# Kernel optimization log

Measured on AMD Instinct MI355X. Metric: run time of the kernel, lower is better.

## Reference

```python
import jax, jax.numpy as jnp
import numpy as np

B, T, N, D = 8, 12, 325, 256
H = 8
HD = D // H
FF = 1024
SCALE = HD ** -0.5
EPS = 1e-5
NEG_INF = jnp.float32(-1e30)


def layernorm(x, w, b):
    mu = jnp.mean(x, axis=-1, keepdims=True)
    var = jnp.mean(jnp.square(x - mu), axis=-1, keepdims=True)
    return (x - mu) * jax.lax.rsqrt(var + EPS) * w + b


def mha(x, wq, bq, wk, bk, wv, bv, wo, bo, mask):
    # x: (G, L, D); mask: (L, L) bool, True = keep, or None
    G, L, _ = x.shape
    q = (x @ wq + bq).reshape(G, L, H, HD)
    k = (x @ wk + bk).reshape(G, L, H, HD)
    v = (x @ wv + bv).reshape(G, L, H, HD)
    scores = jnp.einsum('glhd,gmhd->ghlm', q, k) * SCALE
    if mask is not None:
        scores = jnp.where(mask[None, None], scores, NEG_INF)
    attn = jax.nn.softmax(scores, axis=-1)
    out = jnp.einsum('ghlm,gmhd->glhd', attn, v).reshape(G, L, D)
    return out @ wo + bo


def setup_inputs() -> dict:
    key = jax.random.key(0)
    ks = jax.random.split(key, 16)
    s = 0.02
    inp = {
        'x': jax.random.normal(ks[0], (B, T, N, D), jnp.float32),
        'adj_mask': jax.random.randint(ks[1], (N, N), 0, 2, jnp.int32),
        'sa_wq': jax.random.normal(ks[2], (D, D)) * s, 'sa_bq': jnp.zeros((D,)),
        'sa_wk': jax.random.normal(ks[3], (D, D)) * s, 'sa_bk': jnp.zeros((D,)),
        'sa_wv': jax.random.normal(ks[4], (D, D)) * s, 'sa_bv': jnp.zeros((D,)),
        'sa_wo': jax.random.normal(ks[5], (D, D)) * s, 'sa_bo': jnp.zeros((D,)),
        'sa_ln_w': jnp.ones((D,)), 'sa_ln_b': jnp.zeros((D,)),
        'ta_wq': jax.random.normal(ks[6], (D, D)) * s, 'ta_bq': jnp.zeros((D,)),
        'ta_wk': jax.random.normal(ks[7], (D, D)) * s, 'ta_bk': jnp.zeros((D,)),
        'ta_wv': jax.random.normal(ks[8], (D, D)) * s, 'ta_bv': jnp.zeros((D,)),
        'ta_wo': jax.random.normal(ks[9], (D, D)) * s, 'ta_bo': jnp.zeros((D,)),
        'ta_ln_w': jnp.ones((D,)), 'ta_ln_b': jnp.zeros((D,)),
        'f_w1': jax.random.normal(ks[10], (D, FF)) * s, 'f_b1': jnp.zeros((FF,)),
        'f_w2': jax.random.normal(ks[11], (FF, D)) * s, 'f_b2': jnp.zeros((D,)),
        'f_ln_w': jnp.ones((D,)), 'f_ln_b': jnp.zeros((D,)),
    }
    return inp


def reference(x, adj_mask,
              sa_wq, sa_bq, sa_wk, sa_bk, sa_wv, sa_bv, sa_wo, sa_bo, sa_ln_w, sa_ln_b,
              ta_wq, ta_bq, ta_wk, ta_bk, ta_wv, ta_bv, ta_wo, ta_bo, ta_ln_w, ta_ln_b,
              f_w1, f_b1, f_w2, f_b2, f_ln_w, f_ln_b):
    # Spatial attention over N at each (b, t)
    xs = x.reshape(B * T, N, D)
    sa = mha(xs, sa_wq, sa_bq, sa_wk, sa_bk, sa_wv, sa_bv, sa_wo, sa_bo,
             adj_mask != 0).reshape(B, T, N, D)
    x = layernorm(x + sa, sa_ln_w, sa_ln_b)

    # Temporal attention over T at each (b, n), causal
    xt = x.transpose(0, 2, 1, 3).reshape(B * N, T, D)
    causal = jnp.tril(jnp.ones((T, T), dtype=bool))
    ta = mha(xt, ta_wq, ta_bq, ta_wk, ta_bk, ta_wv, ta_bv, ta_wo, ta_bo, causal)
    ta = ta.reshape(B, N, T, D).transpose(0, 2, 1, 3)
    x = layernorm(x + ta, ta_ln_w, ta_ln_b)

    # FFN with exact GELU (torch nn.GELU default)
    h = jax.nn.gelu(x @ f_w1 + f_b1, approximate=False)
    out = layernorm(x + (h @ f_w2 + f_b2), f_ln_w, f_ln_b)
    return out
```

## Files before the change

### kernel.cpp

```cpp
#include <hip/hip_runtime.h>
#include <hip/hip_bf16.h>
#include <math.h>

#define B_   8
#define T_   12
#define NN   325
#define DD   256
#define HH   8
#define HD   32
#define FFD  1024
#define MTOK (B_*T_*NN)
#define QKVD 768
#define ATT_SCALE 0.17677669529663687f
#define LN_EPS 1e-5f
#define NEG_BIG (-1e30f)

typedef __attribute__((ext_vector_type(8))) __bf16 bf16x8;
typedef __attribute__((ext_vector_type(4))) float  f32x4;
typedef __attribute__((ext_vector_type(4))) short  shortx4;
typedef __attribute__((ext_vector_type(8))) unsigned short ushortx8;

static __device__ inline float bf2f(unsigned short u) {
  union { float f; unsigned int i; } c; c.i = ((unsigned int)u) << 16; return c.f;
}

#if __has_builtin(__builtin_amdgcn_mfma_f32_16x16x16bf16_1k)
#define MFMA16(a,b,c) __builtin_amdgcn_mfma_f32_16x16x16bf16_1k((a),(b),(c),0,0,0)
#else
static __device__ inline f32x4 mfma16_fn(shortx4 a, shortx4 b, f32x4 c) {
  f32x4 d;
  asm volatile("v_mfma_f32_16x16x16_bf16 %0, %1, %2, %3"
               : "=v"(d) : "v"(a), "v"(b), "v"(c));
  return d;
}
#define MFMA16(a,b,c) mfma16_fn((a),(b),(c))
#endif

#define GLDS(gsrc, ldst) \
  __builtin_amdgcn_global_load_lds((const __attribute__((address_space(1))) void*)(gsrc), \
                                   (__attribute__((address_space(3))) void*)(ldst), 16, 0, 0)

__global__ __launch_bounds__(256) void gemm_mfma(
    const __hip_bfloat16* __restrict__ A,
    const __hip_bfloat16* __restrict__ Wt,
    const float* __restrict__ bias,
    float* __restrict__ Cf, __hip_bfloat16* __restrict__ Cb,
    int Mr, int Nr, int Kr, int mode)
{
  __shared__ __hip_bfloat16 As[2][128 * 32];
  __shared__ __hip_bfloat16 Bs[2][128 * 32];

  const int NB  = Nr >> 7;
  const int nwg = gridDim.x;
  const int orig = blockIdx.x;
  const int qq = nwg >> 3, rr = nwg & 7;
  const int xcd = orig & 7, off = orig >> 3;
  const int id = (xcd < rr ? xcd * (qq + 1) : rr * (qq + 1) + (xcd - rr) * qq) + off;
  const int n0 = (id % NB) * 128;
  const int m0 = (id / NB) * 128;

  const int tid  = threadIdx.x;
  const int w    = tid >> 6;
  const int lane = tid & 63;
  const int wr   = w >> 1, wc = w & 1;

  f32x4 acc[4][4] = {};

  const int c4   = lane & 3;
  const int r0   = w * 32 + (lane >> 2);
  const int csw  = (c4 - (r0 >> 1)) & 3;
  const int scol = csw * 8;
  int ar0 = m0 + r0;      if (ar0 >= Mr) ar0 = Mr - 1;
  int ar1 = m0 + r0 + 16; if (ar1 >= Mr) ar1 = Mr - 1;
  const size_t aOff0 = (size_t)ar0 * Kr + scol;
  const size_t aOff1 = (size_t)ar1 * Kr + scol;
  const size_t bOff0 = (size_t)(n0 + r0) * Kr + scol;
  const size_t bOff1 = (size_t)(n0 + r0 + 16) * Kr + scol;

  const int lr = lane & 15;
  const int lg = lane >> 4;
  int offA[4], offB[4];
  #pragma unroll
  for (int i = 0; i < 4; ++i) {
    int rA = wr * 64 + i * 16 + lr;
    offA[i] = rA * 32 + (((lg + (rA >> 1)) & 3) * 8);
    int rB = wc * 64 + i * 16 + lr;
    offB[i] = rB * 32 + (((lg + (rB >> 1)) & 3) * 8);
  }
  const int nk = Kr >> 5;

#define STAGE_T(buf, k0) do { \
    GLDS(&A[aOff0 + (k0)],  &As[buf][(w * 32) * 32]); \
    GLDS(&A[aOff1 + (k0)],  &As[buf][(w * 32 + 16) * 32]); \
    GLDS(&Wt[bOff0 + (k0)], &Bs[buf][(w * 32) * 32]); \
    GLDS(&Wt[bOff1 + (k0)], &Bs[buf][(w * 32 + 16) * 32]); \
  } while (0)

  STAGE_T(0, 0);
  if (nk > 1) STAGE_T(1, 32);

  for (int k = 0; k < nk; ++k) {
    if (k + 1 < nk) asm volatile("s_waitcnt vmcnt(4)" ::: "memory");
    else            asm volatile("s_waitcnt vmcnt(0)" ::: "memory");
    __builtin_amdgcn_s_barrier();

    const int buf = k & 1;
    bf16x8 af[4], bfr[4];
    #pragma unroll
    for (int i = 0; i < 4; ++i) {
      af[i]  = *(const bf16x8*)&As[buf][offA[i]];
      bfr[i] = *(const bf16x8*)&Bs[buf][offB[i]];
    }
    asm volatile("s_waitcnt lgkmcnt(0)" ::: "memory");
    __builtin_amdgcn_sched_barrier(0);
    __builtin_amdgcn_s_barrier();

    if (k + 2 < nk) STAGE_T(buf, (k + 2) * 32);

    #pragma unroll
    for (int i = 0; i < 4; ++i)
      #pragma unroll
      for (int j = 0; j < 4; ++j)
        acc[i][j] = __builtin_amdgcn_mfma_f32_16x16x32_bf16(af[i], bfr[j], acc[i][j], 0, 0, 0);
  }
#undef STAGE_T

  const int rg = lg;
  #pragma unroll
  for (int i = 0; i < 4; ++i) {
    int rowb = m0 + wr * 64 + i * 16 + rg * 4;
    #pragma unroll
    for (int j = 0; j < 4; ++j) {
      int col = n0 + wc * 64 + j * 16 + lr;
      float bv = bias[col];
      #pragma unroll
      for (int q = 0; q < 4; ++q) {
        int gm = rowb + q;
        if (gm >= Mr) continue;
        float c = acc[i][j][q] + bv;
        if (mode == 0) {
          Cf[(size_t)gm * Nr + col] = c;
        } else {
          if (mode == 1) c = 0.5f * c * (1.f + erff(c * 0.70710678118654752f));
          Cb[(size_t)gm * Nr + col] = __float2bfloat16(c);
        }
      }
    }
  }
}

__global__ __launch_bounds__(256) void wt_cvt(
    const float* __restrict__ W, __hip_bfloat16* __restrict__ Wt, int K, int N)
{
  __shared__ float t[32][33];
  const int n0 = blockIdx.x * 32, k0 = blockIdx.y * 32;
  const int tx = threadIdx.x & 31, ty = threadIdx.x >> 5;
  #pragma unroll
  for (int i = 0; i < 32; i += 8)
    t[ty + i][tx] = W[(size_t)(k0 + ty + i) * N + n0 + tx];
  __syncthreads();
  #pragma unroll
  for (int i = 0; i < 32; i += 8)
    Wt[(size_t)(n0 + ty + i) * K + k0 + tx] = __float2bfloat16(t[tx][ty + i]);
}

__global__ __launch_bounds__(256) void cvt_bf16(
    const float* __restrict__ x, __hip_bfloat16* __restrict__ y, int n4)
{
  int i = blockIdx.x * 256 + threadIdx.x;
  if (i >= n4) return;
  float4 v = reinterpret_cast<const float4*>(x)[i];
  union { shortx4 s; __hip_bfloat16 h[4]; } u;
  u.h[0] = __float2bfloat16(v.x); u.h[1] = __float2bfloat16(v.y);
  u.h[2] = __float2bfloat16(v.z); u.h[3] = __float2bfloat16(v.w);
  reinterpret_cast<shortx4*>(y)[i] = u.s;
}

__global__ __launch_bounds__(256) void bias_cat3(
    const float* __restrict__ a, const float* __restrict__ b,
    const float* __restrict__ c, float* __restrict__ o)
{
  int i = blockIdx.x * 256 + threadIdx.x;
  if (i < 256) o[i] = a[i];
  else if (i < 512) o[i] = b[i - 256];
  else if (i < 768) o[i] = c[i - 512];
}

__global__ __launch_bounds__(256) void maskpack(
    const int* __restrict__ adj, unsigned int* __restrict__ mb)
{
  int idx = blockIdx.x * 256 + threadIdx.x;
  if (idx >= NN * 11) return;
  int l = idx / 11, w = idx % 11;
  unsigned int bits = 0;
  #pragma unroll 4
  for (int b = 0; b < 32; ++b) {
    int m = w * 32 + b;
    if (m < NN && adj[l * NN + m] != 0) bits |= (1u << b);
  }
  mb[idx] = bits;
}

__global__ __launch_bounds__(256) void spatial_attn_mfma(
    const __hip_bfloat16* __restrict__ qkv,
    const unsigned int* __restrict__ mb,
    __hip_bfloat16* __restrict__ out)
{
  constexpr int KP = 40;
  constexpr int VP = 340;
  __shared__ unsigned short Kl[336 * KP];
  __shared__ unsigned short Vt[32 * VP];

  const int g = blockIdx.x, h = blockIdx.y;
  const int tid = threadIdx.x;
  const int w = tid >> 6, lane = tid & 63;
  const int lq = lane & 15, lg = lane >> 4;

  const size_t baseQ = (size_t)g * NN * QKVD + (size_t)h * HD;
  const size_t baseK = baseQ + 256;
  const size_t baseV = baseQ + 512;

  for (int idx = tid; idx < 32 * (VP - NN); idx += 256) {
    int d = idx / (VP - NN), kk = NN + idx % (VP - NN);
    Vt[d * VP + kk] = 0;
  }
  for (int idx = tid; idx < NN * 4; idx += 256) {
    int row = idx >> 2, cc = (idx & 3) * 8;
    union { bf16x8 v; unsigned short u[8]; } kv, vv;
    kv.v = *(const bf16x8*)&qkv[baseK + (size_t)row * QKVD + cc];
    *(bf16x8*)&Kl[row * KP + cc] = kv.v;
    vv.v = *(const bf16x8*)&qkv[baseV + (size_t)row * QKVD + cc];
    #pragma unroll
    for (int j = 0; j < 8; ++j) Vt[(cc + j) * VP + row] = vv.u[j];
  }
  __syncthreads();

  for (int qt = w; qt < 21; qt += 4) {
    const int query = qt * 16 + lq;
    const int qc = query < NN ? query : NN - 1;
    const bf16x8 qf = *(const bf16x8*)&qkv[baseQ + (size_t)qc * QKVD + lg * 8];
    const unsigned int* mrow = &mb[qc * 11];

    f32x4 accL = {0.f, 0.f, 0.f, 0.f};
    f32x4 accH = {0.f, 0.f, 0.f, 0.f};
    float mrun = -INFINITY, lrun = 0.f;

    for (int t = 0; t < 21; ++t) {
      bf16x8 kf = *(const bf16x8*)&Kl[(t * 16 + lq) * KP + lg * 8];
      f32x4 st = __builtin_amdgcn_mfma_f32_16x16x32_bf16(
          kf, qf, (f32x4){0.f, 0.f, 0.f, 0.f}, 0, 0, 0);
      const unsigned int mw = mrow[t >> 1];
      const int kbase = t * 16 + lg * 4;
      const int bbase = (t & 1) * 16 + lg * 4;
      float s[4];
      #pragma unroll
      for (int q = 0; q < 4; ++q) {
        float fill = (kbase + q < NN) ? NEG_BIG : -INFINITY;
        s[q] = ((mw >> (bbase + q)) & 1u) ? st[q] * ATT_SCALE : fill;
      }
      float tmax = fmaxf(fmaxf(s[0], s[1]), fmaxf(s[2], s[3]));
      tmax = fmaxf(tmax, __shfl_xor(tmax, 16));
      tmax = fmaxf(tmax, __shfl_xor(tmax, 32));
      const float mnew = fmaxf(mrun, tmax);
      const float corr = __expf(mrun - mnew);
      float p0 = __expf(s[0] - mnew), p1 = __expf(s[1] - mnew);
      float p2 = __expf(s[2] - mnew), p3 = __expf(s[3] - mnew);
      float ps = p0 + p1 + p2 + p3;
      ps += __shfl_xor(ps, 16);
      ps += __shfl_xor(ps, 32);
      lrun = lrun * corr + ps;
      mrun = mnew;
      accL *= corr; accH *= corr;
      union { shortx4 s4; __hip_bfloat16 hh[4]; } up;
      up.hh[0] = __float2bfloat16(p0); up.hh[1] = __float2bfloat16(p1);
      up.hh[2] = __float2bfloat16(p2); up.hh[3] = __float2bfloat16(p3);
      shortx4 vaL = *(const shortx4*)&Vt[lq * VP + kbase];
      shortx4 vaH = *(const shortx4*)&Vt[(lq + 16) * VP + kbase];
      accL = MFMA16(vaL, up.s4, accL);
      accH = MFMA16(vaH, up.s4, accH);
    }

    if (query < NN) {
      const float inv = 1.f / lrun;
      const size_t ob = ((size_t)(g * NN + query)) * DD + (size_t)h * HD;
      union { shortx4 s4; __hip_bfloat16 hh[4]; } uL, uH;
      #pragma unroll
      for (int q = 0; q < 4; ++q) {
        uL.hh[q] = __float2bfloat16(accL[q] * inv);
        uH.hh[q] = __float2bfloat16(accH[q] * inv);
      }
      *(shortx4*)&out[ob + lg * 4]      = uL.s4;
      *(shortx4*)&out[ob + 16 + lg * 4] = uH.s4;
    }
  }
}

__global__ __launch_bounds__(256) void temporal_attn(
    const __hip_bfloat16* __restrict__ qkv, __hip_bfloat16* __restrict__ out)
{
  int idx = blockIdx.x * 256 + threadIdx.x;
  const int total = B_ * NN * HH * T_;
  if (idx >= total) return;

  int t  = idx % T_;
  int h  = (idx / T_) % HH;
  int n  = (idx / (T_ * HH)) % NN;
  int b  = idx / (T_ * HH * NN);

  const size_t tq = (size_t)((b * T_ + t) * NN + n) * QKVD + h * HD;
  float qr[HD];
  #pragma unroll
  for (int c8 = 0; c8 < 4; ++c8) {
    ushortx8 u = *(const ushortx8*)&qkv[tq + c8 * 8];
    #pragma unroll
    for (int j = 0; j < 8; ++j) qr[c8 * 8 + j] = bf2f(u[j]);
  }

  float o[HD] = {};
  float mrun = -INFINITY, lrun = 0.f;

  for (int tt = 0; tt <= t; ++tt) {
    const size_t tk = (size_t)((b * T_ + tt) * NN + n) * QKVD + h * HD;
    float s = 0.f;
    #pragma unroll
    for (int c8 = 0; c8 < 4; ++c8) {
      ushortx8 u = *(const ushortx8*)&qkv[tk + 256 + c8 * 8];
      #pragma unroll
      for (int j = 0; j < 8; ++j) s += qr[c8 * 8 + j] * bf2f(u[j]);
    }
    s *= ATT_SCALE;

    float mnew = fmaxf(mrun, s);
    float corr = __expf(mrun - mnew);
    float p = __expf(s - mnew);
    lrun = lrun * corr + p;
    #pragma unroll
    for (int c8 = 0; c8 < 4; ++c8) {
      ushortx8 u = *(const ushortx8*)&qkv[tk + 512 + c8 * 8];
      #pragma unroll
      for (int j = 0; j < 8; ++j) o[c8 * 8 + j] = o[c8 * 8 + j] * corr + p * bf2f(u[j]);
    }
    mrun = mnew;
  }

  float inv = 1.f / lrun;
  __hip_bfloat16* op = out + ((size_t)((b * T_ + t) * NN + n)) * DD + h * HD;
  #pragma unroll
  for (int d0 = 0; d0 < HD; d0 += 4) {
    union { shortx4 s; __hip_bfloat16 h4[4]; } u;
    #pragma unroll
    for (int j = 0; j < 4; ++j) u.h4[j] = __float2bfloat16(o[d0 + j] * inv);
    *reinterpret_cast<shortx4*>(op + d0) = u.s;
  }
}

__global__ __launch_bounds__(64) void add_ln(
    const float* __restrict__ x, const float* __restrict__ r,
    const float* __restrict__ w, const float* __restrict__ bb,
    float* __restrict__ y, __hip_bfloat16* __restrict__ ybf)
{
  const size_t row = blockIdx.x;
  const int lane = threadIdx.x;

  const float4 xv = reinterpret_cast<const float4*>(x + row * DD)[lane];
  const float4 rv = reinterpret_cast<const float4*>(r + row * DD)[lane];
  float e[4] = {xv.x + rv.x, xv.y + rv.y, xv.z + rv.z, xv.w + rv.w};

  float s  = e[0] + e[1] + e[2] + e[3];
  float ss = e[0]*e[0] + e[1]*e[1] + e[2]*e[2] + e[3]*e[3];
  #pragma unroll
  for (int off = 32; off > 0; off >>= 1) {
    s  += __shfl_xor(s,  off, 64);
    ss += __shfl_xor(ss, off, 64);
  }
  float mu  = s * (1.f / DD);
  float var = ss * (1.f / DD) - mu * mu;
  float rs  = rsqrtf(var + LN_EPS);

  const float4 wv = reinterpret_cast<const float4*>(w)[lane];
  const float4 bv = reinterpret_cast<const float4*>(bb)[lane];
  float o0 = (e[0] - mu) * rs * wv.x + bv.x;
  float o1 = (e[1] - mu) * rs * wv.y + bv.y;
  float o2 = (e[2] - mu) * rs * wv.z + bv.z;
  float o3 = (e[3] - mu) * rs * wv.w + bv.w;
  float4 yv = {o0, o1, o2, o3};
  reinterpret_cast<float4*>(y + row * DD)[lane] = yv;
  if (ybf) {
    union { shortx4 s4; __hip_bfloat16 h4[4]; } u;
    u.h4[0] = __float2bfloat16(o0); u.h4[1] = __float2bfloat16(o1);
    u.h4[2] = __float2bfloat16(o2); u.h4[3] = __float2bfloat16(o3);
    reinterpret_cast<shortx4*>(ybf + row * DD)[lane] = u.s4;
  }
}

extern "C" void kernel_launch(void* const* d_in, const int* in_sizes, int n_in,
                              void* d_out, int out_size, void* d_ws, size_t ws_size,
                              hipStream_t stream)
{
  const float* x0   = (const float*)d_in[0];
  const int*   adj  = (const int*)  d_in[1];
  const float* sa_wq = (const float*)d_in[2];
  const float* sa_bq = (const float*)d_in[3];
  const float* sa_wk = (const float*)d_in[4];
  const float* sa_bk = (const float*)d_in[5];
  const float* sa_wv = (const float*)d_in[6];
  const float* sa_bv = (const float*)d_in[7];
  const float* sa_wo = (const float*)d_in[8];
  const float* sa_bo = (const float*)d_in[9];
  const float* sa_lw = (const float*)d_in[10];
  const float* sa_lb = (const float*)d_in[11];
  const float* ta_wq = (const float*)d_in[12];
  const float* ta_bq = (const float*)d_in[13];
  const float* ta_wk = (const float*)d_in[14];
  const float* ta_bk = (const float*)d_in[15];
  const float* ta_wv = (const float*)d_in[16];
  const float* ta_bv = (const float*)d_in[17];
  const float* ta_wo = (const float*)d_in[18];
  const float* ta_bo = (const float*)d_in[19];
  const float* ta_lw = (const float*)d_in[20];
  const float* ta_lb = (const float*)d_in[21];
  const float* f_w1  = (const float*)d_in[22];
  const float* f_b1  = (const float*)d_in[23];
  const float* f_w2  = (const float*)d_in[24];
  const float* f_b2  = (const float*)d_in[25];
  const float* f_lw  = (const float*)d_in[26];
  const float* f_lb  = (const float*)d_in[27];

  float* out = (float*)d_out;
  float* ws  = (float*)d_ws;

  const size_t P = (size_t)MTOK * DD;
  if (ws_size < 7 * P * sizeof(float)) return;

  float* R0 = ws;
  __hip_bfloat16* QKVb = (__hip_bfloat16*)(ws + P);
  __hip_bfloat16* HIDb = (__hip_bfloat16*)(ws + P);
  float* R3 = ws + 3 * P;
  float* R4 = ws + 4 * P;
  __hip_bfloat16* X0b  = (__hip_bfloat16*)(ws + 5 * P);
  __hip_bfloat16* X1b  = (__hip_bfloat16*)(ws + 5 * P + P / 2);
  __hip_bfloat16* ATTb = (__hip_bfloat16*)(ws + 6 * P);
  __hip_bfloat16* Wb   = (__hip_bfloat16*)(ws + 6 * P + P / 2);

  __hip_bfloat16* sa_qkv_t = Wb;
  __hip_bfloat16* ta_qkv_t = Wb + 196608;
  __hip_bfloat16* sa_wo_t  = Wb + 393216;
  __hip_bfloat16* ta_wo_t  = Wb + 458752;
  __hip_bfloat16* f_w1_t   = Wb + 524288;
  __hip_bfloat16* f_w2_t   = Wb + 786432;
  float* sa_qkvb = (float*)(Wb + 1048576);
  float* ta_qkvb = sa_qkvb + 768;
  unsigned int* MB = (unsigned int*)(ta_qkvb + 768);

  wt_cvt<<<dim3(DD/32, DD/32), 256, 0, stream>>>(sa_wq, sa_qkv_t,          DD, DD);
  wt_cvt<<<dim3(DD/32, DD/32), 256, 0, stream>>>(sa_wk, sa_qkv_t + 65536,  DD, DD);
  wt_cvt<<<dim3(DD/32, DD/32), 256, 0, stream>>>(sa_wv, sa_qkv_t + 131072, DD, DD);
  wt_cvt<<<dim3(DD/32, DD/32), 256, 0, stream>>>(ta_wq, ta_qkv_t,          DD, DD);
  wt_cvt<<<dim3(DD/32, DD/32), 256, 0, stream>>>(ta_wk, ta_qkv_t + 65536,  DD, DD);
  wt_cvt<<<dim3(DD/32, DD/32), 256, 0, stream>>>(ta_wv, ta_qkv_t + 131072, DD, DD);
  wt_cvt<<<dim3(DD/32, DD/32), 256, 0, stream>>>(sa_wo, sa_wo_t, DD, DD);
  wt_cvt<<<dim3(DD/32, DD/32), 256, 0, stream>>>(ta_wo, ta_wo_t, DD, DD);
  wt_cvt<<<dim3(FFD/32, DD/32), 256, 0, stream>>>(f_w1, f_w1_t, DD, FFD);
  wt_cvt<<<dim3(DD/32, FFD/32), 256, 0, stream>>>(f_w2, f_w2_t, FFD, DD);
  bias_cat3<<<3, 256, 0, stream>>>(sa_bq, sa_bk, sa_bv, sa_qkvb);
  bias_cat3<<<3, 256, 0, stream>>>(ta_bq, ta_bk, ta_bv, ta_qkvb);
  maskpack<<<(NN * 11 + 255) / 256, 256, 0, stream>>>(adj, MB);
  {
    int n4 = (int)(P / 4);
    cvt_bf16<<<(n4 + 255) / 256, 256, 0, stream>>>(x0, X0b, n4);
  }

  const int MBk = (MTOK + 127) / 128;
  auto gemm = [&](const __hip_bfloat16* A, const __hip_bfloat16* Wt, const float* bias,
                  float* Cf, __hip_bfloat16* Cb, int Nr, int Kr, int mode) {
    int nwg = (Nr / 128) * MBk;
    gemm_mfma<<<nwg, 256, 0, stream>>>(A, Wt, bias, Cf, Cb, MTOK, Nr, Kr, mode);
  };

  gemm(X0b, sa_qkv_t, sa_qkvb, nullptr, QKVb, QKVD, DD, 2);
  spatial_attn_mfma<<<dim3(B_ * T_, HH), 256, 0, stream>>>(QKVb, MB, ATTb);
  gemm(ATTb, sa_wo_t, sa_bo, R3, nullptr, DD, DD, 0);
  add_ln<<<MTOK, 64, 0, stream>>>(x0, R3, sa_lw, sa_lb, R4, X1b);

  gemm(X1b, ta_qkv_t, ta_qkvb, nullptr, QKVb, QKVD, DD, 2);
  {
    int total = B_ * NN * HH * T_;
    temporal_attn<<<(total + 255) / 256, 256, 0, stream>>>(QKVb, ATTb);
  }
  gemm(ATTb, ta_wo_t, ta_bo, R3, nullptr, DD, DD, 0);
  add_ln<<<MTOK, 64, 0, stream>>>(R4, R3, ta_lw, ta_lb, R0, X0b);

  gemm(X0b, f_w1_t, f_b1, nullptr, HIDb, FFD, DD, 1);
  gemm(HIDb, f_w2_t, f_b2, R3, nullptr, DD, FFD, 0);
  add_ln<<<MTOK, 64, 0, stream>>>(R0, R3, f_lw, f_lb, out, nullptr);
}
```

Before: 413.2 us.

## Load GEMM operands directly from global memory and store projections as bf16

The GEMM drops its LDS double-buffered global_load_lds staging and barriers. Each lane now reads its MFMA fragments straight from global memory through per-row pointers, relying on cache for reuse across waves. The output-projection GEMMs also write bf16 instead of fp32, and add_ln reads the bf16 residual, which cuts store and load traffic. The risks are lost LDS data reuse, more redundant global and cache traffic with poorly coalesced 16-byte loads, and slightly lower precision in the projection outputs.

```diff
diff --git a/kernel.cpp b/kernel.cpp
--- a/kernel.cpp
+++ b/kernel.cpp
@@ -36,20 +36,13 @@
 #define MFMA16(a,b,c) mfma16_fn((a),(b),(c))
 #endif
 
-#define GLDS(gsrc, ldst) \
-  __builtin_amdgcn_global_load_lds((const __attribute__((address_space(1))) void*)(gsrc), \
-                                   (__attribute__((address_space(3))) void*)(ldst), 16, 0, 0)
-
-__global__ __launch_bounds__(256) void gemm_mfma(
+__global__ __launch_bounds__(256) void gemm_direct(
     const __hip_bfloat16* __restrict__ A,
     const __hip_bfloat16* __restrict__ Wt,
     const float* __restrict__ bias,
-    float* __restrict__ Cf, __hip_bfloat16* __restrict__ Cb,
-    int Mr, int Nr, int Kr, int mode)
-{
-  __shared__ __hip_bfloat16 As[2][128 * 32];
-  __shared__ __hip_bfloat16 Bs[2][128 * 32];
-
+    __hip_bfloat16* __restrict__ Cb,
+    int Mr, int Nr, int Kr, int gelu)
+{
   const int NB  = Nr >> 7;
   const int nwg = gridDim.x;
   const int orig = blockIdx.x;
@@ -63,72 +56,40 @@
   const int w    = tid >> 6;
   const int lane = tid & 63;
   const int wr   = w >> 1, wc = w & 1;
+  const int lr   = lane & 15, lg = lane >> 4;
 
   f32x4 acc[4][4] = {};
 
-  const int c4   = lane & 3;
-  const int r0   = w * 32 + (lane >> 2);
-  const int csw  = (c4 - (r0 >> 1)) & 3;
-  const int scol = csw * 8;
-  int ar0 = m0 + r0;      if (ar0 >= Mr) ar0 = Mr - 1;
-  int ar1 = m0 + r0 + 16; if (ar1 >= Mr) ar1 = Mr - 1;
-  const size_t aOff0 = (size_t)ar0 * Kr + scol;
-  const size_t aOff1 = (size_t)ar1 * Kr + scol;
-  const size_t bOff0 = (size_t)(n0 + r0) * Kr + scol;
-  const size_t bOff1 = (size_t)(n0 + r0 + 16) * Kr + scol;
-
-  const int lr = lane & 15;
-  const int lg = lane >> 4;
-  int offA[4], offB[4];
+  const __hip_bfloat16* ap[4];
+  const __hip_bfloat16* bp[4];
   #pragma unroll
   for (int i = 0; i < 4; ++i) {
-    int rA = wr * 64 + i * 16 + lr;
-    offA[i] = rA * 32 + (((lg + (rA >> 1)) & 3) * 8);
-    int rB = wc * 64 + i * 16 + lr;
-    offB[i] = rB * 32 + (((lg + (rB >> 1)) & 3) * 8);
-  }
+    int r = m0 + wr * 64 + i * 16 + lr;
+    if (r >= Mr) r = Mr - 1;
+    ap[i] = A + (size_t)r * Kr + lg * 8;
+    int c = n0 + wc * 64 + i * 16 + lr;
+    bp[i] = Wt + (size_t)c * Kr + lg * 8;
+  }
+
   const int nk = Kr >> 5;
-
-#define STAGE_T(buf, k0) do { \
-    GLDS(&A[aOff0 + (k0)],  &As[buf][(w * 32) * 32]); \
-    GLDS(&A[aOff1 + (k0)],  &As[buf][(w * 32 + 16) * 32]); \
-    GLDS(&Wt[bOff0 + (k0)], &Bs[buf][(w * 32) * 32]); \
-    GLDS(&Wt[bOff1 + (k0)], &Bs[buf][(w * 32 + 16) * 32]); \
-  } while (0)
-
-  STAGE_T(0, 0);
-  if (nk > 1) STAGE_T(1, 32);
-
+  #pragma unroll 2
   for (int k = 0; k < nk; ++k) {
-    if (k + 1 < nk) asm volatile("s_waitcnt vmcnt(4)" ::: "memory");
-    else            asm volatile("s_waitcnt vmcnt(0)" ::: "memory");
-    __builtin_amdgcn_s_barrier();
-
-    const int buf = k & 1;
     bf16x8 af[4], bfr[4];
     #pragma unroll
     for (int i = 0; i < 4; ++i) {
-      af[i]  = *(const bf16x8*)&As[buf][offA[i]];
-      bfr[i] = *(const bf16x8*)&Bs[buf][offB[i]];
-    }
-    asm volatile("s_waitcnt lgkmcnt(0)" ::: "memory");
-    __builtin_amdgcn_sched_barrier(0);
-    __builtin_amdgcn_s_barrier();
-
-    if (k + 2 < nk) STAGE_T(buf, (k + 2) * 32);
-
+      af[i]  = *(const bf16x8*)(ap[i] + k * 32);
+      bfr[i] = *(const bf16x8*)(bp[i] + k * 32);
+    }
     #pragma unroll
     for (int i = 0; i < 4; ++i)
       #pragma unroll
       for (int j = 0; j < 4; ++j)
         acc[i][j] = __builtin_amdgcn_mfma_f32_16x16x32_bf16(af[i], bfr[j], acc[i][j], 0, 0, 0);
   }
-#undef STAGE_T
-
-  const int rg = lg;
+
   #pragma unroll
   for (int i = 0; i < 4; ++i) {
-    int rowb = m0 + wr * 64 + i * 16 + rg * 4;
+    int rowb = m0 + wr * 64 + i * 16 + lg * 4;
     #pragma unroll
     for (int j = 0; j < 4; ++j) {
       int col = n0 + wc * 64 + j * 16 + lr;
@@ -138,12 +99,8 @@
         int gm = rowb + q;
         if (gm >= Mr) continue;
         float c = acc[i][j][q] + bv;
-        if (mode == 0) {
-          Cf[(size_t)gm * Nr + col] = c;
-        } else {
-          if (mode == 1) c = 0.5f * c * (1.f + erff(c * 0.70710678118654752f));
-          Cb[(size_t)gm * Nr + col] = __float2bfloat16(c);
-        }
+        if (gelu) c = 0.5f * c * (1.f + erff(c * 0.70710678118654752f));
+        Cb[(size_t)gm * Nr + col] = __float2bfloat16(c);
       }
     }
   }
@@ -355,7 +312,7 @@
 }
 
 __global__ __launch_bounds__(64) void add_ln(
-    const float* __restrict__ x, const float* __restrict__ r,
+    const float* __restrict__ x, const __hip_bfloat16* __restrict__ r,
     const float* __restrict__ w, const float* __restrict__ bb,
     float* __restrict__ y, __hip_bfloat16* __restrict__ ybf)
 {
@@ -363,8 +320,10 @@
   const int lane = threadIdx.x;
 
   const float4 xv = reinterpret_cast<const float4*>(x + row * DD)[lane];
-  const float4 rv = reinterpret_cast<const float4*>(r + row * DD)[lane];
-  float e[4] = {xv.x + rv.x, xv.y + rv.y, xv.z + rv.z, xv.w + rv.w};
+  union { shortx4 s4; unsigned short u[4]; } rv;
+  rv.s4 = reinterpret_cast<const shortx4*>(r + row * DD)[lane];
+  float e[4] = {xv.x + bf2f(rv.u[0]), xv.y + bf2f(rv.u[1]),
+                xv.z + bf2f(rv.u[2]), xv.w + bf2f(rv.u[3])};
 
   float s  = e[0] + e[1] + e[2] + e[3];
   float ss = e[0]*e[0] + e[1]*e[1] + e[2]*e[2] + e[3]*e[3];
@@ -435,7 +394,7 @@
   float* R0 = ws;
   __hip_bfloat16* QKVb = (__hip_bfloat16*)(ws + P);
   __hip_bfloat16* HIDb = (__hip_bfloat16*)(ws + P);
-  float* R3 = ws + 3 * P;
+  __hip_bfloat16* PRJ  = (__hip_bfloat16*)(ws + 3 * P);
   float* R4 = ws + 4 * P;
   __hip_bfloat16* X0b  = (__hip_bfloat16*)(ws + 5 * P);
   __hip_bfloat16* X1b  = (__hip_bfloat16*)(ws + 5 * P + P / 2);
@@ -472,25 +431,25 @@
 
   const int MBk = (MTOK + 127) / 128;
   auto gemm = [&](const __hip_bfloat16* A, const __hip_bfloat16* Wt, const float* bias,
-                  float* Cf, __hip_bfloat16* Cb, int Nr, int Kr, int mode) {
+                  __hip_bfloat16* Cb, int Nr, int Kr, int gelu) {
     int nwg = (Nr / 128) * MBk;
-    gemm_mfma<<<nwg, 256, 0, stream>>>(A, Wt, bias, Cf, Cb, MTOK, Nr, Kr, mode);
+    gemm_direct<<<nwg, 256, 0, stream>>>(A, Wt, bias, Cb, MTOK, Nr, Kr, gelu);
   };
 
-  gemm(X0b, sa_qkv_t, sa_qkvb, nullptr, QKVb, QKVD, DD, 2);
+  gemm(X0b, sa_qkv_t, sa_qkvb, QKVb, QKVD, DD, 0);
   spatial_attn_mfma<<<dim3(B_ * T_, HH), 256, 0, stream>>>(QKVb, MB, ATTb);
-  gemm(ATTb, sa_wo_t, sa_bo, R3, nullptr, DD, DD, 0);
-  add_ln<<<MTOK, 64, 0, stream>>>(x0, R3, sa_lw, sa_lb, R4, X1b);
-
-  gemm(X1b, ta_qkv_t, ta_qkvb, nullptr, QKVb, QKVD, DD, 2);
+  gemm(ATTb, sa_wo_t, sa_bo, PRJ, DD, DD, 0);
+  add_ln<<<MTOK, 64, 0, stream>>>(x0, PRJ, sa_lw, sa_lb, R4, X1b);
+
+  gemm(X1b, ta_qkv_t, ta_qkvb, QKVb, QKVD, DD, 0);
   {
     int total = B_ * NN * HH * T_;
     temporal_attn<<<(total + 255) / 256, 256, 0, stream>>>(QKVb, ATTb);
   }
-  gemm(ATTb, ta_wo_t, ta_bo, R3, nullptr, DD, DD, 0);
-  add_ln<<<MTOK, 64, 0, stream>>>(R4, R3, ta_lw, ta_lb, R0, X0b);
-
-  gemm(X0b, f_w1_t, f_b1, nullptr, HIDb, FFD, DD, 1);
-  gemm(HIDb, f_w2_t, f_b2, R3, nullptr, DD, FFD, 0);
-  add_ln<<<MTOK, 64, 0, stream>>>(R0, R3, f_lw, f_lb, out, nullptr);
-}
+  gemm(ATTb, ta_wo_t, ta_bo, PRJ, DD, DD, 0);
+  add_ln<<<MTOK, 64, 0, stream>>>(R4, PRJ, ta_lw, ta_lb, R0, X0b);
+
+  gemm(X0b, f_w1_t, f_b1, HIDb, FFD, DD, 1);
+  gemm(HIDb, f_w2_t, f_b2, PRJ, DD, FFD, 0);
+  add_ln<<<MTOK, 64, 0, stream>>>(R0, PRJ, f_lw, f_lb, out, nullptr);
+}
```

After: 509.4 us. +23.3%, slower.

## Add K=256 GEMM with resident weight slab and bf16 projection outputs

Applied to the files above, without the earlier changes.

Adds a GEMM kernel for K=256 projections in which each workgroup keeps a 64-column slice of the weight matrix resident in LDS. It then loops over four 128-row M tiles, reading A fragments directly from global memory without LDS staging. The output projections now write bf16 instead of fp32, and add_ln reads bf16 residuals, which halves that traffic at some cost in precision. The K=1024 FFN2 GEMM keeps the old double-buffered kernel, specialized to bf16 output.

```diff
diff --git a/kernel.cpp b/kernel.cpp
--- a/kernel.cpp
+++ b/kernel.cpp
@@ -40,12 +40,98 @@
   __builtin_amdgcn_global_load_lds((const __attribute__((address_space(1))) void*)(gsrc), \
                                    (__attribute__((address_space(3))) void*)(ldst), 16, 0, 0)
 
-__global__ __launch_bounds__(256) void gemm_mfma(
+__global__ __launch_bounds__(256) void gemm_persist(
     const __hip_bfloat16* __restrict__ A,
     const __hip_bfloat16* __restrict__ Wt,
     const float* __restrict__ bias,
-    float* __restrict__ Cf, __hip_bfloat16* __restrict__ Cb,
-    int Mr, int Nr, int Kr, int mode)
+    __hip_bfloat16* __restrict__ Cb,
+    int Mr, int Nr, int gelu)
+{
+  constexpr int KR = 256;
+  constexpr int BP = 264;
+  __shared__ __hip_bfloat16 Bs[64 * BP];
+
+  const int NS  = Nr >> 6;
+  const int nwg = gridDim.x;
+  const int orig = blockIdx.x;
+  const int qq = nwg >> 3, rr = nwg & 7;
+  const int xcd = orig & 7, off = orig >> 3;
+  const int id = (xcd < rr ? xcd * (qq + 1) : rr * (qq + 1) + (xcd - rr) * qq) + off;
+  const int n0 = (id % NS) * 64;
+  const int mg = id / NS;
+
+  const int tid = threadIdx.x;
+  const int w = tid >> 6, lane = tid & 63;
+  const int wr = w >> 1, wc = w & 1;
+  const int lr = lane & 15, lg = lane >> 4;
+
+  for (int u = tid; u < 64 * 32; u += 256) {
+    int row = u >> 5, c8 = (u & 31) * 8;
+    bf16x8 v = *(const bf16x8*)&Wt[(size_t)(n0 + row) * KR + c8];
+    *(bf16x8*)&Bs[row * BP + c8] = v;
+  }
+  __syncthreads();
+
+  int offB[2];
+  #pragma unroll
+  for (int j = 0; j < 2; ++j) offB[j] = (wc * 32 + j * 16 + lr) * BP;
+
+  float bv[2];
+  #pragma unroll
+  for (int j = 0; j < 2; ++j) bv[j] = bias[n0 + wc * 32 + j * 16 + lr];
+
+  #pragma unroll 1
+  for (int mt = 0; mt < 4; ++mt) {
+    const int mbase = (mg * 4 + mt) * 128;
+    const __hip_bfloat16* ap[4];
+    #pragma unroll
+    for (int i = 0; i < 4; ++i) {
+      int r = mbase + wr * 64 + i * 16 + lr;
+      if (r >= Mr) r = Mr - 1;
+      ap[i] = A + (size_t)r * KR + lg * 8;
+    }
+
+    f32x4 acc[4][2] = {};
+    #pragma unroll
+    for (int k = 0; k < 8; ++k) {
+      bf16x8 af[4], bfr[2];
+      #pragma unroll
+      for (int i = 0; i < 4; ++i) af[i] = *(const bf16x8*)(ap[i] + k * 32);
+      #pragma unroll
+      for (int j = 0; j < 2; ++j)
+        bfr[j] = *(const bf16x8*)&Bs[offB[j] + k * 32 + lg * 8];
+      #pragma unroll
+      for (int i = 0; i < 4; ++i)
+        #pragma unroll
+        for (int j = 0; j < 2; ++j)
+          acc[i][j] = __builtin_amdgcn_mfma_f32_16x16x32_bf16(af[i], bfr[j], acc[i][j], 0, 0, 0);
+    }
+
+    #pragma unroll
+    for (int i = 0; i < 4; ++i) {
+      int rowb = mbase + wr * 64 + i * 16 + lg * 4;
+      #pragma unroll
+      for (int j = 0; j < 2; ++j) {
+        int col = n0 + wc * 32 + j * 16 + lr;
+        #pragma unroll
+        for (int q = 0; q < 4; ++q) {
+          int gm = rowb + q;
+          if (gm >= Mr) continue;
+          float c = acc[i][j][q] + bv[j];
+          if (gelu) c = 0.5f * c * (1.f + erff(c * 0.70710678118654752f));
+          Cb[(size_t)gm * Nr + col] = __float2bfloat16(c);
+        }
+      }
+    }
+  }
+}
+
+__global__ __launch_bounds__(256) void gemm_k1024(
+    const __hip_bfloat16* __restrict__ A,
+    const __hip_bfloat16* __restrict__ Wt,
+    const float* __restrict__ bias,
+    __hip_bfloat16* __restrict__ Cb,
+    int Mr, int Nr, int Kr)
 {
   __shared__ __hip_bfloat16 As[2][128 * 32];
   __shared__ __hip_bfloat16 Bs[2][128 * 32];
@@ -125,10 +211,9 @@
   }
 #undef STAGE_T
 
-  const int rg = lg;
   #pragma unroll
   for (int i = 0; i < 4; ++i) {
-    int rowb = m0 + wr * 64 + i * 16 + rg * 4;
+    int rowb = m0 + wr * 64 + i * 16 + lg * 4;
     #pragma unroll
     for (int j = 0; j < 4; ++j) {
       int col = n0 + wc * 64 + j * 16 + lr;
@@ -137,13 +222,7 @@
       for (int q = 0; q < 4; ++q) {
         int gm = rowb + q;
         if (gm >= Mr) continue;
-        float c = acc[i][j][q] + bv;
-        if (mode == 0) {
-          Cf[(size_t)gm * Nr + col] = c;
-        } else {
-          if (mode == 1) c = 0.5f * c * (1.f + erff(c * 0.70710678118654752f));
-          Cb[(size_t)gm * Nr + col] = __float2bfloat16(c);
-        }
+        Cb[(size_t)gm * Nr + col] = __float2bfloat16(acc[i][j][q] + bv);
       }
     }
   }
@@ -355,7 +434,7 @@
 }
 
 __global__ __launch_bounds__(64) void add_ln(
-    const float* __restrict__ x, const float* __restrict__ r,
+    const float* __restrict__ x, const __hip_bfloat16* __restrict__ r,
     const float* __restrict__ w, const float* __restrict__ bb,
     float* __restrict__ y, __hip_bfloat16* __restrict__ ybf)
 {
@@ -363,8 +442,10 @@
   const int lane = threadIdx.x;
 
   const float4 xv = reinterpret_cast<const float4*>(x + row * DD)[lane];
-  const float4 rv = reinterpret_cast<const float4*>(r + row * DD)[lane];
-  float e[4] = {xv.x + rv.x, xv.y + rv.y, xv.z + rv.z, xv.w + rv.w};
+  union { shortx4 s4; unsigned short u[4]; } rv;
+  rv.s4 = reinterpret_cast<const shortx4*>(r + row * DD)[lane];
+  float e[4] = {xv.x + bf2f(rv.u[0]), xv.y + bf2f(rv.u[1]),
+                xv.z + bf2f(rv.u[2]), xv.w + bf2f(rv.u[3])};
 
   float s  = e[0] + e[1] + e[2] + e[3];
   float ss = e[0]*e[0] + e[1]*e[1] + e[2]*e[2] + e[3]*e[3];
@@ -435,7 +516,7 @@
   float* R0 = ws;
   __hip_bfloat16* QKVb = (__hip_bfloat16*)(ws + P);
   __hip_bfloat16* HIDb = (__hip_bfloat16*)(ws + P);
-  float* R3 = ws + 3 * P;
+  __hip_bfloat16* PRJ  = (__hip_bfloat16*)(ws + 3 * P);
   float* R4 = ws + 4 * P;
   __hip_bfloat16* X0b  = (__hip_bfloat16*)(ws + 5 * P);
   __hip_bfloat16* X1b  = (__hip_bfloat16*)(ws + 5 * P + P / 2);
@@ -470,27 +551,29 @@
     cvt_bf16<<<(n4 + 255) / 256, 256, 0, stream>>>(x0, X0b, n4);
   }
 
-  const int MBk = (MTOK + 127) / 128;
-  auto gemm = [&](const __hip_bfloat16* A, const __hip_bfloat16* Wt, const float* bias,
-                  float* Cf, __hip_bfloat16* Cb, int Nr, int Kr, int mode) {
-    int nwg = (Nr / 128) * MBk;
-    gemm_mfma<<<nwg, 256, 0, stream>>>(A, Wt, bias, Cf, Cb, MTOK, Nr, Kr, mode);
+  auto gemmP = [&](const __hip_bfloat16* A, const __hip_bfloat16* Wt, const float* bias,
+                   __hip_bfloat16* Cb, int Nr, int gelu) {
+    int nwg = (Nr / 64) * 61;
+    gemm_persist<<<nwg, 256, 0, stream>>>(A, Wt, bias, Cb, MTOK, Nr, gelu);
   };
 
-  gemm(X0b, sa_qkv_t, sa_qkvb, nullptr, QKVb, QKVD, DD, 2);
+  gemmP(X0b, sa_qkv_t, sa_qkvb, QKVb, QKVD, 0);
   spatial_attn_mfma<<<dim3(B_ * T_, HH), 256, 0, stream>>>(QKVb, MB, ATTb);
-  gemm(ATTb, sa_wo_t, sa_bo, R3, nullptr, DD, DD, 0);
-  add_ln<<<MTOK, 64, 0, stream>>>(x0, R3, sa_lw, sa_lb, R4, X1b);
-
-  gemm(X1b, ta_qkv_t, ta_qkvb, nullptr, QKVb, QKVD, DD, 2);
+  gemmP(ATTb, sa_wo_t, sa_bo, PRJ, DD, 0);
+  add_ln<<<MTOK, 64, 0, stream>>>(x0, PRJ, sa_lw, sa_lb, R4, X1b);
+
+  gemmP(X1b, ta_qkv_t, ta_qkvb, QKVb, QKVD, 0);
   {
     int total = B_ * NN * HH * T_;
     temporal_attn<<<(total + 255) / 256, 256, 0, stream>>>(QKVb, ATTb);
   }
-  gemm(ATTb, ta_wo_t, ta_bo, R3, nullptr, DD, DD, 0);
-  add_ln<<<MTOK, 64, 0, stream>>>(R4, R3, ta_lw, ta_lb, R0, X0b);
-
-  gemm(X0b, f_w1_t, f_b1, nullptr, HIDb, FFD, DD, 1);
-  gemm(HIDb, f_w2_t, f_b2, R3, nullptr, DD, FFD, 0);
-  add_ln<<<MTOK, 64, 0, stream>>>(R0, R3, f_lw, f_lb, out, nullptr);
-}
+  gemmP(ATTb, ta_wo_t, ta_bo, PRJ, DD, 0);
+  add_ln<<<MTOK, 64, 0, stream>>>(R4, PRJ, ta_lw, ta_lb, R0, X0b);
+
+  gemmP(X0b, f_w1_t, f_b1, HIDb, FFD, 1);
+  {
+    int nwg = (DD / 128) * 244;
+    gemm_k1024<<<nwg, 256, 0, stream>>>(HIDb, f_w2_t, f_b2, PRJ, MTOK, DD, FFD);
+  }
+  add_ln<<<MTOK, 64, 0, stream>>>(R0, PRJ, f_lw, f_lb, out, nullptr);
+}
```

Measured after the change: 456.7 us. +10.5%, slower.
